# Kernel optimization log

Hardware: AMD Instinct MI355X
Metric: run time of the kernel (lower is better)

The kernel has to match this reference:

```python
import jax, jax.numpy as jnp
import numpy as np

D_MODEL = 1024
NUM_HEADS = 16
D_K = D_MODEL // NUM_HEADS
D_FF = 4096
EPS = 1e-5


def _layernorm(x, gamma, beta):
    mu = jnp.mean(x, axis=-1, keepdims=True)
    var = jnp.mean(jnp.square(x - mu), axis=-1, keepdims=True)
    return (x - mu) * jax.lax.rsqrt(var + EPS) * gamma + beta


def setup_inputs() -> dict:
    key = jax.random.key(0)
    ks = jax.random.split(key, 16)
    B, S = 4, 2048
    s_in = 1.0 / np.sqrt(D_MODEL)
    s_ff = 1.0 / np.sqrt(D_FF)
    inp = {
        "x": jax.random.normal(ks[0], (B, S, D_MODEL), jnp.float32),
        "src_mask": jnp.ones((B, 1, 1, S), jnp.int32),
        "w_q": jax.random.normal(ks[1], (D_MODEL, D_MODEL), jnp.float32) * s_in,
        "b_q": jnp.zeros((D_MODEL,), jnp.float32),
        "w_k": jax.random.normal(ks[2], (D_MODEL, D_MODEL), jnp.float32) * s_in,
        "b_k": jnp.zeros((D_MODEL,), jnp.float32),
        "w_v": jax.random.normal(ks[3], (D_MODEL, D_MODEL), jnp.float32) * s_in,
        "b_v": jnp.zeros((D_MODEL,), jnp.float32),
        "w_o": jax.random.normal(ks[4], (D_MODEL, D_MODEL), jnp.float32) * s_in,
        "b_o": jnp.zeros((D_MODEL,), jnp.float32),
        "w1": jax.random.normal(ks[5], (D_MODEL, D_FF), jnp.float32) * s_in,
        "b1": jnp.zeros((D_FF,), jnp.float32),
        "w2": jax.random.normal(ks[6], (D_FF, D_MODEL), jnp.float32) * s_ff,
        "b2": jnp.zeros((D_MODEL,), jnp.float32),
        "g1": jnp.ones((D_MODEL,), jnp.float32),
        "be1": jnp.zeros((D_MODEL,), jnp.float32),
        "g2": jnp.ones((D_MODEL,), jnp.float32),
        "be2": jnp.zeros((D_MODEL,), jnp.float32),
    }
    return inp


def reference(x, src_mask, w_q, b_q, w_k, b_k, w_v, b_v, w_o, b_o,
              w1, b1, w2, b2, g1, be1, g2, be2):
    B, S, _ = x.shape

    def split_heads(t):  # [B,S,D] -> [B,H,S,dk]
        return t.reshape(B, S, NUM_HEADS, D_K).transpose(0, 2, 1, 3)

    q = split_heads(x @ w_q + b_q)
    k = split_heads(x @ w_k + b_k)
    v = split_heads(x @ w_v + b_v)

    scores = jnp.einsum("bhqd,bhkd->bhqk", q, k) / np.sqrt(D_K)
    scores = jnp.where(src_mask == 0, -jnp.inf, scores)
    attn = jax.nn.softmax(scores, axis=-1)
    ctx = jnp.einsum("bhqk,bhkd->bhqd", attn, v)
    merged = ctx.transpose(0, 2, 1, 3).reshape(B, S, D_MODEL)
    attn_out = merged @ w_o + b_o

    h = _layernorm(x + attn_out, g1, be1)
    ff = jax.nn.relu(h @ w1 + b1) @ w2 + b2
    return _layernorm(h + ff, g2, be2)
```

## Files before the change

kernel.cpp:

```cpp
#include <hip/hip_runtime.h>

typedef unsigned short u16;
typedef __attribute__((ext_vector_type(4))) unsigned short u16x4;
typedef __attribute__((ext_vector_type(8))) short bf16x8;
typedef __attribute__((ext_vector_type(4))) float f32x4;
typedef __attribute__((ext_vector_type(16))) float f32x16;

__device__ inline float bf2f(u16 u) {
  union { unsigned int i; float f; } v; v.i = ((unsigned int)u) << 16; return v.f;
}
__device__ inline u16 f2bf(float f) {
  union { float f; unsigned int i; } v; v.f = f;
  unsigned int r = v.i + 0x7fffu + ((v.i >> 16) & 1u);
  return (u16)(r >> 16);
}
__device__ inline unsigned int cvt_pk_bf16(float lo, float hi) {
  unsigned int r;
  asm("v_cvt_pk_bf16_f32 %0, %1, %2" : "=v"(r) : "v"(lo), "v"(hi));
  return r;
}
__device__ inline f32x16 zero16() {
  f32x16 z;
  #pragma unroll
  for (int i = 0; i < 16; ++i) z[i] = 0.f;
  return z;
}

typedef const __attribute__((address_space(1))) unsigned int* gas_t;
typedef __attribute__((address_space(3))) unsigned int* las_t;
__device__ inline void gload_lds16(const u16* g, u16* l) {
  __builtin_amdgcn_global_load_lds((gas_t)(unsigned long long)(const void*)g,
                                   (las_t)(unsigned int)(unsigned long long)(void*)l,
                                   16, 0, 0);
}

__global__ __launch_bounds__(256) void cvt_bf16(const float* __restrict__ src,
                                                u16* __restrict__ dst, int n) {
  int i = (blockIdx.x * 256 + threadIdx.x) * 4;
  if (i >= n) return;
  float4 v = *(const float4*)(src + i);
  u16x4 o;
  o.x = f2bf(v.x); o.y = f2bf(v.y); o.z = f2bf(v.z); o.w = f2bf(v.w);
  *(u16x4*)(dst + i) = o;
}

__global__ __launch_bounds__(256) void concat3(const float* __restrict__ a,
                                               const float* __restrict__ b,
                                               const float* __restrict__ c,
                                               float* __restrict__ o, int n) {
  int i = blockIdx.x * 256 + threadIdx.x;
  if (i >= n) return;
  o[i] = a[i]; o[n + i] = b[i]; o[2 * n + i] = c[i];
}

__global__ __launch_bounds__(256) void transpose_f32_bf16(const float* __restrict__ src,
                                                          u16* __restrict__ dst,
                                                          int R, int C) {
  __shared__ u16 tile[32][33];
  int tx = threadIdx.x & 31, ty = threadIdx.x >> 5;
  int c0 = blockIdx.x * 32, r0 = blockIdx.y * 32;
  #pragma unroll
  for (int i = ty; i < 32; i += 8)
    tile[i][tx] = f2bf(src[(size_t)(r0 + i) * C + c0 + tx]);
  __syncthreads();
  #pragma unroll
  for (int i = ty; i < 32; i += 8)
    dst[(size_t)(c0 + i) * R + r0 + tx] = tile[tx][i];
}

__global__ __launch_bounds__(256) void transpose_v(const u16* __restrict__ src,
                                                   u16* __restrict__ VT,
                                                   int B, int S, int H, int RS, int CO) {
  __shared__ u16 tile[32][33];
  int tx = threadIdx.x & 31, ty = threadIdx.x >> 5;
  int s0 = blockIdx.x * 32, d0 = blockIdx.y * 32;
  int bh = blockIdx.z;
  int b = bh / H, h = bh % H;
  #pragma unroll
  for (int i = ty; i < 32; i += 8)
    tile[i][tx] = src[(size_t)(b * S + s0 + i) * RS + CO + h * 64 + d0 + tx];
  __syncthreads();
  #pragma unroll
  for (int i = ty; i < 32; i += 8)
    VT[((size_t)bh * 64 + d0 + i) * S + s0 + tx] = tile[tx][i];
}

__global__ __launch_bounds__(256) void gemm_bt(const u16* __restrict__ A,
                                               const u16* __restrict__ Bt,
                                               const float* __restrict__ bias,
                                               u16* __restrict__ C,
                                               int M, int N, int K, int relu) {
  __shared__ u16 As[128 * 32];
  __shared__ u16 Bs[128 * 32];
  const int tid = threadIdx.x;
  const int lane = tid & 63, wid = tid >> 6;
  const int lr = lane & 15, quad = lane >> 4;
  const int wm = (wid >> 1) * 64, wn = (wid & 1) * 64;
  const int m0 = blockIdx.y * 128, n0 = blockIdx.x * 128;
  const int lrow = lane >> 2;
  const int lcol = (lane & 3) * 8;

  f32x4 acc[4][4];
  const f32x4 zero = {0.f, 0.f, 0.f, 0.f};
  #pragma unroll
  for (int mt = 0; mt < 4; ++mt)
    #pragma unroll
    for (int nt = 0; nt < 4; ++nt) acc[mt][nt] = zero;

  for (int k0 = 0; k0 < K; k0 += 32) {
    #pragma unroll
    for (int it = 0; it < 2; ++it) {
      int rbase = wid * 32 + it * 16;
      gload_lds16(A + (size_t)(m0 + rbase + lrow) * K + k0 + lcol, &As[rbase * 32]);
      gload_lds16(Bt + (size_t)(n0 + rbase + lrow) * K + k0 + lcol, &Bs[rbase * 32]);
    }
    __syncthreads();
    bf16x8 af[4], bfr[4];
    #pragma unroll
    for (int mt = 0; mt < 4; ++mt)
      af[mt] = *(const bf16x8*)(&As[(wm + mt * 16 + lr) * 32 + quad * 8]);
    #pragma unroll
    for (int nt = 0; nt < 4; ++nt)
      bfr[nt] = *(const bf16x8*)(&Bs[(wn + nt * 16 + lr) * 32 + quad * 8]);
    #pragma unroll
    for (int mt = 0; mt < 4; ++mt)
      #pragma unroll
      for (int nt = 0; nt < 4; ++nt)
        acc[mt][nt] = __builtin_amdgcn_mfma_f32_16x16x32_bf16(af[mt], bfr[nt], acc[mt][nt], 0, 0, 0);
    __syncthreads();
  }

  #pragma unroll
  for (int nt = 0; nt < 4; ++nt) {
    int n = n0 + wn + nt * 16 + lr;
    float bv = bias[n];
    #pragma unroll
    for (int mt = 0; mt < 4; ++mt) {
      #pragma unroll
      for (int i = 0; i < 4; ++i) {
        int m = m0 + wm + mt * 16 + quad * 4 + i;
        float v = acc[mt][nt][i] + bv;
        if (relu) v = fmaxf(v, 0.f);
        C[(size_t)m * N + n] = f2bf(v);
      }
    }
  }
}

__global__ __launch_bounds__(256) void flash_attn(const u16* __restrict__ Qp,
                                                  const u16* __restrict__ Kp,
                                                  const u16* __restrict__ VT,
                                                  const int* __restrict__ mask,
                                                  u16* __restrict__ ctx,
                                                  int B, int S, int H, int QSTR) {
  __shared__ u16 kt_lds[64 * 64];
  __shared__ u16 vt_lds[64 * 64];
  const int tid = threadIdx.x;
  const int lane = tid & 63, wid = tid >> 6;
  const int l31 = lane & 31, hi = lane >> 5;
  const int bh = blockIdx.y;
  const int b = bh / H, h = bh % H;
  const u16* vt_base = VT + (size_t)bh * 64 * S;
  const int* mbase = mask + b * S;
  const float SC = 0.125f * 1.44269504089f;

  const int srl = lane >> 3;
  const int scol = ((lane & 7) ^ srl) * 8;
  const int rsw = (lane & 7) << 3;

  const int q = blockIdx.x * 128 + wid * 32 + l31;
  bf16x8 qf[4];
  {
    const u16* qptr = Qp + (size_t)(b * S + q) * QSTR + h * 64;
    #pragma unroll
    for (int t = 0; t < 4; ++t)
      qf[t] = *(const bf16x8*)(qptr + t * 16 + hi * 8);
  }

  float m_i = -1e30f, l_i = 0.f;
  f32x16 o0 = zero16(), o1 = zero16();

  const u16* kgp = Kp + ((size_t)b * S + wid * 16 + srl) * QSTR + h * 64 + scol;
  const u16* vgp = vt_base + (size_t)(wid * 16 + srl) * S + scol;
  u16* klb = &kt_lds[(wid * 16) * 64];
  u16* vlb = &vt_lds[(wid * 16) * 64];

  for (int kt = 0; kt < S; kt += 64) {
    gload_lds16(kgp + (size_t)kt * QSTR, klb);
    gload_lds16(kgp + (size_t)(kt + 8) * QSTR, klb + 8 * 64);
    gload_lds16(vgp + kt, vlb);
    gload_lds16(vgp + 8 * (size_t)S + kt, vlb + 8 * 64);
    int mv = mbase[kt + lane];
    unsigned long long bal = __ballot(mv != 0);
    __syncthreads();

    f32x16 sa0 = zero16(), sa1 = zero16();
    const u16* krow0 = &kt_lds[l31 * 64];
    const u16* krow1 = &kt_lds[(32 + l31) * 64];
    __builtin_amdgcn_s_setprio(1);
    #pragma unroll
    for (int dblock = 0; dblock < 4; ++dblock) {
      int c = (dblock * 16 + hi * 8) ^ rsw;
      bf16x8 kf0 = *(const bf16x8*)(krow0 + c);
      bf16x8 kf1 = *(const bf16x8*)(krow1 + c);
      sa0 = __builtin_amdgcn_mfma_f32_32x32x16_bf16(kf0, qf[dblock], sa0, 0, 0, 0);
      sa1 = __builtin_amdgcn_mfma_f32_32x32x16_bf16(kf1, qf[dblock], sa1, 0, 0, 0);
    }
    __builtin_amdgcn_s_setprio(0);

    if (bal != 0xFFFFFFFFFFFFFFFFull) {
      unsigned long long balh = bal >> (hi * 4);
      #pragma unroll
      for (int r = 0; r < 16; ++r) {
        int kloc = (r & 3) + 8 * (r >> 2);
        if (!((balh >> kloc) & 1)) sa0[r] = -2e30f;
        if (!((balh >> (32 + kloc)) & 1)) sa1[r] = -2e30f;
      }
    }

    float tmax = sa0[0];
    #pragma unroll
    for (int r = 1; r < 16; ++r) tmax = fmaxf(tmax, sa0[r]);
    #pragma unroll
    for (int r = 0; r < 16; ++r) tmax = fmaxf(tmax, sa1[r]);
    tmax = fmaxf(tmax, __shfl_xor(tmax, 32, 64));
    if (__any(tmax > m_i + 44.0f)) {
      float mn = fmaxf(m_i, tmax);
      float al = exp2f((m_i - mn) * SC);
      m_i = mn;
      l_i *= al;
      #pragma unroll
      for (int r = 0; r < 16; ++r) { o0[r] *= al; o1[r] *= al; }
    }
    float msc = m_i * SC;
    float rs = 0.f;
    #pragma unroll
    for (int r = 0; r < 16; ++r) {
      float p0 = exp2f(__builtin_fmaf(sa0[r], SC, -msc));
      float p1 = exp2f(__builtin_fmaf(sa1[r], SC, -msc));
      sa0[r] = p0; sa1[r] = p1; rs += p0 + p1;
    }
    l_i += rs;

    unsigned pfw[4][4];
    #pragma unroll
    for (int b1 = 0; b1 < 2; ++b1) {
      #pragma unroll
      for (int pair = 0; pair < 2; ++pair) {
        unsigned X0 = cvt_pk_bf16(sa0[(2 * b1) * 4 + pair * 2], sa0[(2 * b1) * 4 + pair * 2 + 1]);
        unsigned Y0 = cvt_pk_bf16(sa0[(2 * b1 + 1) * 4 + pair * 2], sa0[(2 * b1 + 1) * 4 + pair * 2 + 1]);
        unsigned Xp0 = __shfl_xor(X0, 32, 64);
        unsigned Yp0 = __shfl_xor(Y0, 32, 64);
        pfw[b1][pair] = hi ? Yp0 : X0;
        pfw[b1][pair + 2] = hi ? Y0 : Xp0;
        unsigned X1 = cvt_pk_bf16(sa1[(2 * b1) * 4 + pair * 2], sa1[(2 * b1) * 4 + pair * 2 + 1]);
        unsigned Y1 = cvt_pk_bf16(sa1[(2 * b1 + 1) * 4 + pair * 2], sa1[(2 * b1 + 1) * 4 + pair * 2 + 1]);
        unsigned Xp1 = __shfl_xor(X1, 32, 64);
        unsigned Yp1 = __shfl_xor(Y1, 32, 64);
        pfw[2 + b1][pair] = hi ? Yp1 : X1;
        pfw[2 + b1][pair + 2] = hi ? Y1 : Xp1;
      }
    }

    const u16* vrow0 = &vt_lds[l31 * 64];
    const u16* vrow1 = &vt_lds[(32 + l31) * 64];
    __builtin_amdgcn_s_setprio(1);
    #pragma unroll
    for (int kb = 0; kb < 4; ++kb) {
      int c = (kb * 16 + hi * 8) ^ rsw;
      bf16x8 vf0 = *(const bf16x8*)(vrow0 + c);
      bf16x8 vf1 = *(const bf16x8*)(vrow1 + c);
      union { unsigned w[4]; bf16x8 v; } pu;
      pu.w[0] = pfw[kb][0]; pu.w[1] = pfw[kb][1];
      pu.w[2] = pfw[kb][2]; pu.w[3] = pfw[kb][3];
      o0 = __builtin_amdgcn_mfma_f32_32x32x16_bf16(vf0, pu.v, o0, 0, 0, 0);
      o1 = __builtin_amdgcn_mfma_f32_32x32x16_bf16(vf1, pu.v, o1, 0, 0, 0);
    }
    __builtin_amdgcn_s_setprio(0);
    __syncthreads();
  }

  l_i += __shfl_xor(l_i, 32, 64);
  float linv = 1.f / fmaxf(l_i, 1e-30f);
  u16* op = ctx + (size_t)(b * S + q) * (H * 64) + h * 64;
  #pragma unroll
  for (int rq = 0; rq < 4; ++rq) {
    uint2 w0, w1;
    w0.x = cvt_pk_bf16(o0[rq * 4 + 0] * linv, o0[rq * 4 + 1] * linv);
    w0.y = cvt_pk_bf16(o0[rq * 4 + 2] * linv, o0[rq * 4 + 3] * linv);
    *(uint2*)(op + rq * 8 + hi * 4) = w0;
    w1.x = cvt_pk_bf16(o1[rq * 4 + 0] * linv, o1[rq * 4 + 1] * linv);
    w1.y = cvt_pk_bf16(o1[rq * 4 + 2] * linv, o1[rq * 4 + 3] * linv);
    *(uint2*)(op + 32 + rq * 8 + hi * 4) = w1;
  }
}

__device__ inline float block_reduce_sum(float v, float* sbuf) {
  #pragma unroll
  for (int m = 1; m < 64; m <<= 1) v += __shfl_xor(v, m, 64);
  int w = threadIdx.x >> 6;
  if ((threadIdx.x & 63) == 0) sbuf[w] = v;
  __syncthreads();
  v = sbuf[0] + sbuf[1] + sbuf[2] + sbuf[3];
  __syncthreads();
  return v;
}

__global__ __launch_bounds__(256) void add_ln(const float* __restrict__ a32,
                                              const u16* __restrict__ a16,
                                              const u16* __restrict__ b,
                                              const float* __restrict__ g,
                                              const float* __restrict__ be,
                                              u16* __restrict__ out16,
                                              float* __restrict__ out32, int D) {
  __shared__ float sbuf[4];
  int row = blockIdx.x;
  size_t base = (size_t)row * D;
  int i = threadIdx.x * 4;
  float v[4];
  {
    u16x4 bv = *(const u16x4*)(b + base + i);
    if (a32) {
      float4 av = *(const float4*)(a32 + base + i);
      v[0] = av.x + bf2f(bv.x); v[1] = av.y + bf2f(bv.y);
      v[2] = av.z + bf2f(bv.z); v[3] = av.w + bf2f(bv.w);
    } else {
      u16x4 av = *(const u16x4*)(a16 + base + i);
      v[0] = bf2f(av.x) + bf2f(bv.x); v[1] = bf2f(av.y) + bf2f(bv.y);
      v[2] = bf2f(av.z) + bf2f(bv.z); v[3] = bf2f(av.w) + bf2f(bv.w);
    }
  }
  float sum = v[0] + v[1] + v[2] + v[3];
  sum = block_reduce_sum(sum, sbuf);
  float mean = sum / (float)D;
  float var = 0.f;
  #pragma unroll
  for (int j = 0; j < 4; ++j) { float d = v[j] - mean; var += d * d; }
  var = block_reduce_sum(var, sbuf);
  float rstd = rsqrtf(var / (float)D + 1e-5f);
  float4 gv = *(const float4*)(g + i);
  float4 bev = *(const float4*)(be + i);
  float o0 = (v[0] - mean) * rstd * gv.x + bev.x;
  float o1 = (v[1] - mean) * rstd * gv.y + bev.y;
  float o2 = (v[2] - mean) * rstd * gv.z + bev.z;
  float o3 = (v[3] - mean) * rstd * gv.w + bev.w;
  if (out32) {
    float4 o = {o0, o1, o2, o3};
    *(float4*)(out32 + base + i) = o;
  } else {
    u16x4 o;
    o.x = f2bf(o0); o.y = f2bf(o1); o.z = f2bf(o2); o.w = f2bf(o3);
    *(u16x4*)(out16 + base + i) = o;
  }
}

extern "C" void kernel_launch(void* const* d_in, const int* in_sizes, int n_in,
                              void* d_out, int out_size, void* d_ws, size_t ws_size,
                              hipStream_t stream) {
  (void)in_sizes; (void)n_in; (void)out_size; (void)ws_size;
  const float* x   = (const float*)d_in[0];
  const int* mask  = (const int*)d_in[1];
  const float* wq  = (const float*)d_in[2];
  const float* bq  = (const float*)d_in[3];
  const float* wk  = (const float*)d_in[4];
  const float* bk  = (const float*)d_in[5];
  const float* wv  = (const float*)d_in[6];
  const float* bv  = (const float*)d_in[7];
  const float* wo  = (const float*)d_in[8];
  const float* bo  = (const float*)d_in[9];
  const float* w1  = (const float*)d_in[10];
  const float* b1  = (const float*)d_in[11];
  const float* w2  = (const float*)d_in[12];
  const float* b2  = (const float*)d_in[13];
  const float* g1  = (const float*)d_in[14];
  const float* be1 = (const float*)d_in[15];
  const float* g2  = (const float*)d_in[16];
  const float* be2 = (const float*)d_in[17];

  const int B = 4, S = 2048, D = 1024, H = 16, DFF = 4096;
  const int D3 = 3 * D;
  const size_t TOK = (size_t)B * S;
  const size_t TD = TOK * D;

  u16* ws   = (u16*)d_ws;
  u16* QKVp = ws;
  u16* xb   = ws + 3 * TD;
  u16* VT   = xb;
  u16* CTX  = ws + 4 * TD;
  u16* ATT  = ws + 5 * TD;
  u16* Hb   = ws + 6 * TD;
  u16* QKVT = ws + 7 * TD;
  u16* WOT  = QKVT + 3 * (size_t)D * D;
  u16* W1T  = WOT + (size_t)D * D;
  u16* FF1  = ws;
  u16* FF2  = ATT;
  u16* W2T  = QKVT;
  float* biasc = (float*)CTX;

  dim3 blk(256);

  cvt_bf16<<<dim3((unsigned)(TD / (256 * 4))), blk, 0, stream>>>(x, xb, (int)TD);
  concat3<<<dim3(4), blk, 0, stream>>>(bq, bk, bv, biasc, D);

  transpose_f32_bf16<<<dim3(D / 32, D / 32), blk, 0, stream>>>(wq, QKVT, D, D);
  transpose_f32_bf16<<<dim3(D / 32, D / 32), blk, 0, stream>>>(wk, QKVT + (size_t)D * D, D, D);
  transpose_f32_bf16<<<dim3(D / 32, D / 32), blk, 0, stream>>>(wv, QKVT + 2 * (size_t)D * D, D, D);
  transpose_f32_bf16<<<dim3(D / 32, D / 32), blk, 0, stream>>>(wo, WOT, D, D);
  transpose_f32_bf16<<<dim3(DFF / 32, D / 32), blk, 0, stream>>>(w1, W1T, D, DFF);

  gemm_bt<<<dim3(D3 / 128, TOK / 128), blk, 0, stream>>>(xb, QKVT, biasc, QKVp, (int)TOK, D3, D, 0);

  transpose_v<<<dim3(S / 32, 2, B * H), blk, 0, stream>>>(QKVp, VT, B, S, H, D3, 2 * D);

  flash_attn<<<dim3(S / 128, B * H), blk, 0, stream>>>(QKVp, QKVp + D, VT, mask, CTX, B, S, H, D3);

  gemm_bt<<<dim3(D / 128, TOK / 128), blk, 0, stream>>>(CTX, WOT, bo, ATT, (int)TOK, D, D, 0);

  transpose_f32_bf16<<<dim3(D / 32, DFF / 32), blk, 0, stream>>>(w2, W2T, DFF, D);

  add_ln<<<dim3((unsigned)TOK), blk, 0, stream>>>(x, (const u16*)nullptr, ATT, g1, be1,
                                                  Hb, (float*)nullptr, D);

  gemm_bt<<<dim3(DFF / 128, TOK / 128), blk, 0, stream>>>(Hb, W1T, b1, FF1, (int)TOK, DFF, D, 1);
  gemm_bt<<<dim3(D / 128, TOK / 128), blk, 0, stream>>>(FF1, W2T, b2, FF2, (int)TOK, D, DFF, 0);

  add_ln<<<dim3((unsigned)TOK), blk, 0, stream>>>((const float*)nullptr, Hb, FF2, g2, be2,
                                                  (u16*)nullptr, (float*)d_out, D);
}
```

Before: 657.8 us.

## Deepen GEMM K-tile to 64 with swizzled LDS and shrink attention blocks

The GEMM now loads a 64-wide K slice per iteration into XOR-swizzled shared memory and runs two MFMA sub-steps per barrier pair. This halves the number of barriers and is meant to avoid LDS bank conflicts. Flash attention switches to 128-thread blocks covering 64 queries, with a flattened 1D grid that interleaves batch-heads across consecutive blocks. That doubles the block count for better CU occupancy, at the cost of each wave loading more of the K/V tile.

```diff
diff --git a/kernel.cpp b/kernel.cpp
--- a/kernel.cpp
+++ b/kernel.cpp
@@ -90,15 +90,16 @@
                                                const float* __restrict__ bias,
                                                u16* __restrict__ C,
                                                int M, int N, int K, int relu) {
-  __shared__ u16 As[128 * 32];
-  __shared__ u16 Bs[128 * 32];
+  __shared__ u16 As[128 * 64];
+  __shared__ u16 Bs[128 * 64];
   const int tid = threadIdx.x;
   const int lane = tid & 63, wid = tid >> 6;
   const int lr = lane & 15, quad = lane >> 4;
   const int wm = (wid >> 1) * 64, wn = (wid & 1) * 64;
   const int m0 = blockIdx.y * 128, n0 = blockIdx.x * 128;
-  const int lrow = lane >> 2;
-  const int lcol = (lane & 3) * 8;
+  const int grow = lane >> 3;
+  const int gcol = ((lane & 7) ^ grow) * 8;
+  const int rsw = (lr & 7) << 3;
 
   f32x4 acc[4][4];
   const f32x4 zero = {0.f, 0.f, 0.f, 0.f};
@@ -107,26 +108,29 @@
     #pragma unroll
     for (int nt = 0; nt < 4; ++nt) acc[mt][nt] = zero;
 
-  for (int k0 = 0; k0 < K; k0 += 32) {
-    #pragma unroll
-    for (int it = 0; it < 2; ++it) {
-      int rbase = wid * 32 + it * 16;
-      gload_lds16(A + (size_t)(m0 + rbase + lrow) * K + k0 + lcol, &As[rbase * 32]);
-      gload_lds16(Bt + (size_t)(n0 + rbase + lrow) * K + k0 + lcol, &Bs[rbase * 32]);
+  for (int k0 = 0; k0 < K; k0 += 64) {
+    #pragma unroll
+    for (int it = 0; it < 4; ++it) {
+      int rbase = wid * 32 + it * 8;
+      gload_lds16(A + (size_t)(m0 + rbase + grow) * K + k0 + gcol, &As[rbase * 64]);
+      gload_lds16(Bt + (size_t)(n0 + rbase + grow) * K + k0 + gcol, &Bs[rbase * 64]);
     }
     __syncthreads();
-    bf16x8 af[4], bfr[4];
-    #pragma unroll
-    for (int mt = 0; mt < 4; ++mt)
-      af[mt] = *(const bf16x8*)(&As[(wm + mt * 16 + lr) * 32 + quad * 8]);
-    #pragma unroll
-    for (int nt = 0; nt < 4; ++nt)
-      bfr[nt] = *(const bf16x8*)(&Bs[(wn + nt * 16 + lr) * 32 + quad * 8]);
-    #pragma unroll
-    for (int mt = 0; mt < 4; ++mt)
+    #pragma unroll
+    for (int kk = 0; kk < 2; ++kk) {
+      bf16x8 af[4], bfr[4];
+      #pragma unroll
+      for (int mt = 0; mt < 4; ++mt)
+        af[mt] = *(const bf16x8*)(&As[(wm + mt * 16 + lr) * 64 + ((kk * 32 + quad * 8) ^ rsw)]);
       #pragma unroll
       for (int nt = 0; nt < 4; ++nt)
-        acc[mt][nt] = __builtin_amdgcn_mfma_f32_16x16x32_bf16(af[mt], bfr[nt], acc[mt][nt], 0, 0, 0);
+        bfr[nt] = *(const bf16x8*)(&Bs[(wn + nt * 16 + lr) * 64 + ((kk * 32 + quad * 8) ^ rsw)]);
+      #pragma unroll
+      for (int mt = 0; mt < 4; ++mt)
+        #pragma unroll
+        for (int nt = 0; nt < 4; ++nt)
+          acc[mt][nt] = __builtin_amdgcn_mfma_f32_16x16x32_bf16(af[mt], bfr[nt], acc[mt][nt], 0, 0, 0);
+    }
     __syncthreads();
   }
 
@@ -147,7 +151,7 @@
   }
 }
 
-__global__ __launch_bounds__(256) void flash_attn(const u16* __restrict__ Qp,
+__global__ __launch_bounds__(128) void flash_attn(const u16* __restrict__ Qp,
                                                   const u16* __restrict__ Kp,
                                                   const u16* __restrict__ VT,
                                                   const int* __restrict__ mask,
@@ -158,7 +162,9 @@
   const int tid = threadIdx.x;
   const int lane = tid & 63, wid = tid >> 6;
   const int l31 = lane & 31, hi = lane >> 5;
-  const int bh = blockIdx.y;
+  const int bid = blockIdx.x;
+  const int bh = (bid & 7) * 8 + ((bid >> 3) & 7);
+  const int qb = bid >> 6;
   const int b = bh / H, h = bh % H;
   const u16* vt_base = VT + (size_t)bh * 64 * S;
   const int* mbase = mask + b * S;
@@ -168,7 +174,7 @@
   const int scol = ((lane & 7) ^ srl) * 8;
   const int rsw = (lane & 7) << 3;
 
-  const int q = blockIdx.x * 128 + wid * 32 + l31;
+  const int q = qb * 64 + wid * 32 + l31;
   bf16x8 qf[4];
   {
     const u16* qptr = Qp + (size_t)(b * S + q) * QSTR + h * 64;
@@ -180,16 +186,17 @@
   float m_i = -1e30f, l_i = 0.f;
   f32x16 o0 = zero16(), o1 = zero16();
 
-  const u16* kgp = Kp + ((size_t)b * S + wid * 16 + srl) * QSTR + h * 64 + scol;
-  const u16* vgp = vt_base + (size_t)(wid * 16 + srl) * S + scol;
-  u16* klb = &kt_lds[(wid * 16) * 64];
-  u16* vlb = &vt_lds[(wid * 16) * 64];
+  const u16* kgp = Kp + ((size_t)b * S + wid * 32 + srl) * QSTR + h * 64 + scol;
+  const u16* vgp = vt_base + (size_t)(wid * 32 + srl) * S + scol;
+  u16* klb = &kt_lds[(wid * 32) * 64];
+  u16* vlb = &vt_lds[(wid * 32) * 64];
 
   for (int kt = 0; kt < S; kt += 64) {
-    gload_lds16(kgp + (size_t)kt * QSTR, klb);
-    gload_lds16(kgp + (size_t)(kt + 8) * QSTR, klb + 8 * 64);
-    gload_lds16(vgp + kt, vlb);
-    gload_lds16(vgp + 8 * (size_t)S + kt, vlb + 8 * 64);
+    #pragma unroll
+    for (int it = 0; it < 4; ++it) {
+      gload_lds16(kgp + (size_t)(kt + it * 8) * QSTR, klb + it * 8 * 64);
+      gload_lds16(vgp + (size_t)(it * 8) * S + kt, vlb + it * 8 * 64);
+    }
     int mv = mbase[kt + lane];
     unsigned long long bal = __ballot(mv != 0);
     __syncthreads();
@@ -412,7 +419,8 @@
 
   transpose_v<<<dim3(S / 32, 2, B * H), blk, 0, stream>>>(QKVp, VT, B, S, H, D3, 2 * D);
 
-  flash_attn<<<dim3(S / 128, B * H), blk, 0, stream>>>(QKVp, QKVp + D, VT, mask, CTX, B, S, H, D3);
+  flash_attn<<<dim3((unsigned)((S / 64) * B * H)), dim3(128), 0, stream>>>(
+      QKVp, QKVp + D, VT, mask, CTX, B, S, H, D3);
 
   gemm_bt<<<dim3(D / 128, TOK / 128), blk, 0, stream>>>(CTX, WOT, bo, ATT, (int)TOK, D, D, 0);
 
```

Result: no change. 650.0 us (-1.2%).
